# Performance work log

Measured on AMD Instinct MI355X. Metric: run time of the kernel, lower is better.

## Reference

```python
import jax, jax.numpy as jnp
import numpy as np

B, S, D = 2, 2048, 1024
H = 16
HD = D // H
RANK = 8
ALPHA = 8.0
NEG = -1e9


def setup_inputs() -> dict:
    key = jax.random.key(0)
    ks = jax.random.split(key, 7)
    inv = 1.0 / np.sqrt(D)
    return {
        "x": jax.random.normal(ks[0], (B, S, D), dtype=jnp.float32),
        "W_qkv": jax.random.normal(ks[1], (D, 3 * D), dtype=jnp.float32) * inv,
        "b_qkv": jax.random.normal(ks[2], (3 * D,), dtype=jnp.float32) * 0.02,
        # LoRA: A ~ N(0, 1/rank) per torch init; B is zeros at init but given
        # small values here so the LoRA path is exercised numerically.
        "A_lora": jax.random.normal(ks[3], (D, RANK), dtype=jnp.float32) / np.sqrt(RANK),
        "B_lora": jax.random.normal(ks[4], (RANK, 3 * D), dtype=jnp.float32) * 0.02,
        "W_proj": jax.random.normal(ks[5], (D, D), dtype=jnp.float32) * inv,
        "b_proj": jax.random.normal(ks[6], (D,), dtype=jnp.float32) * 0.02,
    }


def _split_heads(t):
    # [B, S, D] -> [B, H, S, HD]
    return t.reshape(B, S, H, HD).transpose(0, 2, 1, 3)


def reference(x, W_qkv, b_qkv, A_lora, B_lora, W_proj, b_proj):
    # c_attn: LoRALayer -> base linear + alpha * (x @ A @ B)
    qkv = x @ W_qkv + b_qkv + (x @ A_lora @ B_lora) * ALPHA  # [B, S, 3D]
    q, k, v = jnp.split(qkv, 3, axis=-1)
    q, k, v = _split_heads(q), _split_heads(k), _split_heads(v)

    # SelfAttentionFunction: QK^T, add mask, THEN divide by sqrt(head_dim)
    causal = jnp.tril(jnp.ones((S, S), dtype=bool))
    mask = jnp.where(causal, 0.0, NEG).astype(x.dtype)  # [S, S] additive
    scores = (jnp.einsum("bhqd,bhkd->bhqk", q, k) + mask) / jnp.sqrt(
        jnp.asarray(HD, dtype=x.dtype)
    )
    attn = jax.nn.softmax(scores, axis=-1)  # [B, H, S, S]
    ctx = jnp.einsum("bhqk,bhkd->bhqd", attn, v)  # [B, H, S, HD]

    # merge heads -> c_proj (plain LoRaLinear: x @ W + b)
    ctx = ctx.transpose(0, 2, 1, 3).reshape(B, S, D)
    out = ctx @ W_proj + b_proj
    return out
```

## Files before the change

kernel.cpp:

```cpp
#include <hip/hip_runtime.h>
#include <hip/hip_bf16.h>


#define BB    2
#define SS    2048
#define DD    1024
#define HH    16
#define HDIM  64
#define N3    3072
#define MR    4096

typedef short short8 __attribute__((ext_vector_type(8)));
typedef short s16x4 __attribute__((ext_vector_type(4)));
typedef float f32x4 __attribute__((ext_vector_type(4)));

#define MFMA16(a, b, c) __builtin_amdgcn_mfma_f32_16x16x32_bf16((a), (b), (c), 0, 0, 0)

__device__ __forceinline__ float b2f(short s) {
    union { unsigned int u; float f; } c;
    c.u = ((unsigned int)(unsigned short)s) << 16;
    return c.f;
}
__device__ __forceinline__ short f2b(float f) {
    union { __hip_bfloat16 h; short s; } c;
    c.h = __float2bfloat16(f);
    return c.s;
}
struct HiLo { short hi, lo; };
__device__ __forceinline__ HiLo split2(float v) {
    HiLo r;
    r.hi = f2b(v);
    r.lo = f2b(v - b2f(r.hi));
    return r;
}

__device__ __forceinline__ void gl_lds16(const void* g, void* l) {
    __builtin_amdgcn_global_load_lds(
        (const __attribute__((address_space(1))) void*)g,
        (__attribute__((address_space(3))) void*)l, 16, 0, 0);
}


__global__ __launch_bounds__(256) void split_x(const float* __restrict__ X,
                                               short* __restrict__ Xhi,
                                               short* __restrict__ Xlo) {
    int kc = blockIdx.x, p = blockIdx.y;
    int tid = threadIdx.x;
    int row = tid >> 1, half = tid & 1;
    const float* src = &X[((size_t)p * 128 + row) * 1024 + kc * 32 + half * 16];
    f32x4 v[4];
#pragma unroll
    for (int u = 0; u < 4; u++) v[u] = *(const f32x4*)(src + u * 4);
    size_t base = ((size_t)p * 32 + kc) * 4096 + (size_t)(half * 2) * 1024 + row * 8;
#pragma unroll
    for (int u = 0; u < 2; u++) {
        short8 h8, l8;
#pragma unroll
        for (int j = 0; j < 8; j++) {
            HiLo hl = split2(v[u * 2 + (j >> 2)][j & 3]);
            h8[j] = hl.hi; l8[j] = hl.lo;
        }
        *(short8*)&Xhi[base + u * 1024] = h8;
        *(short8*)&Xlo[base + u * 1024] = l8;
    }
}

__global__ __launch_bounds__(256) void prep_kernel(
    const float* __restrict__ W, const float* __restrict__ Al,
    const float* __restrict__ Bl, short* __restrict__ Whi,
    short* __restrict__ Wlo, int N, int lora)
{
    __shared__ float sw[64][68];
    __shared__ float sa[64][8];
    __shared__ float sb[8][64];
    int tid = threadIdx.x;
    int n0 = blockIdx.x * 64, k0 = blockIdx.y * 64;
#pragma unroll
    for (int p = 0; p < 4; p++) {
        int idx = p * 256 + tid;
        int kr = idx >> 4, ch = idx & 15;
        *(f32x4*)&sw[kr][ch * 4] = *(const f32x4*)&W[(size_t)(k0 + kr) * N + n0 + ch * 4];
    }
    if (lora) {
        if (tid < 64) {
#pragma unroll
            for (int r = 0; r < 8; r++) sa[tid][r] = Al[(k0 + tid) * 8 + r];
        } else if (tid < 128) {
            int c = tid - 64;
#pragma unroll
            for (int r = 0; r < 8; r++) sb[r][c] = Bl[(size_t)r * N + n0 + c];
        }
    }
    __syncthreads();
#pragma unroll
    for (int p = 0; p < 2; p++) {
        int idx = p * 256 + tid;
        int nr = idx >> 3, ch = idx & 7;
        short8 h8, l8;
#pragma unroll
        for (int j = 0; j < 8; j++) {
            int k = ch * 8 + j;
            float v = sw[k][nr];
            if (lora) {
                float a2 = 0.f;
#pragma unroll
                for (int r = 0; r < 8; r++) a2 += sa[k][r] * sb[r][nr];
                v += 8.0f * a2;
            }
            HiLo hl = split2(v);
            h8[j] = hl.hi;
            l8[j] = hl.lo;
        }
        int n = n0 + nr;
        int kchunk = (k0 >> 5) + (ch >> 2);
        size_t off = ((size_t)(n >> 7) * 32 + kchunk) * 4096 +
                     (size_t)(ch & 3) * 1024 + (n & 127) * 8;
        *(short8*)&Whi[off] = h8;
        *(short8*)&Wlo[off] = l8;
    }
}

__global__ __launch_bounds__(256) void gemm3(
    const short* __restrict__ Ahi, const short* __restrict__ Alo,
    const short* __restrict__ Bhi, const short* __restrict__ Blo,
    const float* __restrict__ bias,
    float* __restrict__ qf, short* __restrict__ khi, short* __restrict__ klo,
    short* __restrict__ vt, float* __restrict__ outf32, int N, int mode)
{
    __shared__ short lds[4][4][128][8];
    int tid = threadIdx.x;
    int wav = tid >> 6, lane = tid & 63;
    int l15 = lane & 15, q4 = lane >> 4;
    int wm = wav & 1, wn = wav >> 1;
    int n0 = blockIdx.x * 128, m0 = blockIdx.y * 128;

    const short* ga_h = Ahi + ((size_t)blockIdx.y * 32) * 4096 + tid * 8;
    const short* ga_l = Alo + ((size_t)blockIdx.y * 32) * 4096 + tid * 8;
    const short* gb_h = Bhi + ((size_t)blockIdx.x * 32) * 4096 + tid * 8;
    const short* gb_l = Blo + ((size_t)blockIdx.x * 32) * 4096 + tid * 8;
    short* l0 = &lds[0][0][0][0] + tid * 8;

    f32x4 acc[4][4] = {};

    for (int kc = 0; kc < 32; ++kc) {
        __syncthreads();
        int koff = kc * 4096;
        gl_lds16(ga_h + koff,        l0);
        gl_lds16(ga_h + koff + 2048, l0 + 2048);
        gl_lds16(ga_l + koff,        l0 + 4096);
        gl_lds16(ga_l + koff + 2048, l0 + 6144);
        gl_lds16(gb_h + koff,        l0 + 8192);
        gl_lds16(gb_h + koff + 2048, l0 + 10240);
        gl_lds16(gb_l + koff,        l0 + 12288);
        gl_lds16(gb_l + koff + 2048, l0 + 14336);
        __syncthreads();
        short8 ah[4], al_[4], bh[4], bl[4];
#pragma unroll
        for (int i = 0; i < 4; i++) {
            ah[i]  = *(short8*)&lds[0][q4][wm * 64 + i * 16 + l15][0];
            al_[i] = *(short8*)&lds[1][q4][wm * 64 + i * 16 + l15][0];
            bh[i]  = *(short8*)&lds[2][q4][wn * 64 + i * 16 + l15][0];
            bl[i]  = *(short8*)&lds[3][q4][wn * 64 + i * 16 + l15][0];
        }
#pragma unroll
        for (int mi = 0; mi < 4; mi++)
#pragma unroll
            for (int ni = 0; ni < 4; ni++) {
                acc[mi][ni] = MFMA16(ah[mi], bh[ni], acc[mi][ni]);
                acc[mi][ni] = MFMA16(ah[mi], bl[ni], acc[mi][ni]);
                acc[mi][ni] = MFMA16(al_[mi], bh[ni], acc[mi][ni]);
            }
    }
#pragma unroll
    for (int ni = 0; ni < 4; ni++) {
        int n = n0 + wn * 64 + ni * 16 + l15;
        float bv = bias[n];
#pragma unroll
        for (int mi = 0; mi < 4; mi++) {
            int mbase = m0 + wm * 64 + mi * 16 + q4 * 4;
#pragma unroll
            for (int r = 0; r < 4; r++) {
                int m = mbase + r;
                float v = acc[mi][ni][r] + bv;
                if (mode != 0) {
                    outf32[(size_t)m * 1024 + n] = v;
                } else if (n0 < 1024) {
                    qf[(size_t)m * 1024 + n] = v * 0.125f;
                } else if (n0 < 2048) {
                    int kk = n - 1024, hh = kk >> 6, hd = kk & 63;
                    int bb_ = m >> 11, s = m & 2047;
                    int oct = hd >> 3;
                    size_t base = ((size_t)((bb_ << 4) + hh) * 32 + (s >> 6)) * 4096
                                  + (size_t)oct * 512 + ((s & 63) ^ oct) * 8 + (hd & 7);
                    HiLo hl = split2(v);
                    khi[base] = hl.hi;
                    klo[base] = hl.lo;
                } else {
                    int kk = n - 2048, hh = kk >> 6, hd = kk & 63;
                    int bb_ = m >> 11, s = m & 2047;
                    int oct = (s >> 3) & 7;
                    size_t base = ((size_t)((bb_ << 4) + hh) * 32 + (s >> 6)) * 4096
                                  + (size_t)oct * 512 + (hd ^ oct) * 8 + (s & 7);
                    vt[base] = f2b(v);
                }
            }
        }
    }
}

__global__ __launch_bounds__(256) void attn_mfma(const float* __restrict__ qf,
                                                 const short* __restrict__ khi,
                                                 const short* __restrict__ klo,
                                                 const short* __restrict__ vtg,
                                                 short* __restrict__ ctxhi,
                                                 short* __restrict__ ctxlo) {
    __shared__ short KhL[2][4096];
    __shared__ short KlL[2][4096];
    __shared__ short VtL[2][4096];
    __shared__ short Pt[4][8][17][8];

    int h = blockIdx.y, b = blockIdx.z;
    int tid = threadIdx.x, wav = tid >> 6, lane = tid & 63;
    int l15 = lane & 15, q4 = lane >> 4;
    const float* bq = qf + (size_t)b * SS * 1024;
    size_t hb = (size_t)((b * 16 + h) * 32) * 4096;
    const short* gkh = khi + hb;
    const short* gkl = klo + hb;
    const short* gvt = vtg + hb;
    int t8 = tid * 8;

#define ISSUE(c, buf)                                                   \
    {                                                                   \
        size_t co_ = (size_t)(c) * 4096 + t8;                           \
        gl_lds16(gkh + co_,        &KhL[buf][t8]);                      \
        gl_lds16(gkh + co_ + 2048, &KhL[buf][t8 + 2048]);               \
        gl_lds16(gkl + co_,        &KlL[buf][t8]);                      \
        gl_lds16(gkl + co_ + 2048, &KlL[buf][t8 + 2048]);               \
        gl_lds16(gvt + co_,        &VtL[buf][t8]);                      \
        gl_lds16(gvt + co_ + 2048, &VtL[buf][t8 + 2048]);               \
    }

    for (int t = 0; t < 2; ++t) {
        int qt = t ? (int)blockIdx.x : 31 - (int)blockIdx.x;
        int qb = qt * 64;

        size_t qoff = (size_t)(qb + wav * 16 + l15) * 1024 + h * 64;
        short8 q0h, q0l, q1h, q1l;
        {
            f32x4 a0 = *(const f32x4*)&bq[qoff + q4 * 8];
            f32x4 a1 = *(const f32x4*)&bq[qoff + q4 * 8 + 4];
            f32x4 c0 = *(const f32x4*)&bq[qoff + 32 + q4 * 8];
            f32x4 c1 = *(const f32x4*)&bq[qoff + 32 + q4 * 8 + 4];
#pragma unroll
            for (int j = 0; j < 4; j++) {
                HiLo u = split2(a0[j]); q0h[j] = u.hi; q0l[j] = u.lo;
                HiLo v = split2(a1[j]); q0h[4 + j] = v.hi; q0l[4 + j] = v.lo;
                HiLo w = split2(c0[j]); q1h[j] = w.hi; q1l[j] = w.lo;
                HiLo z = split2(c1[j]); q1h[4 + j] = z.hi; q1l[4 + j] = z.lo;
            }
        }

        f32x4 o[4] = {};
        float msc = -1e30f;
        float lsc = 0.f;
        int nch = qt + 1;

        ISSUE(0, 0);
        __syncthreads();

        for (int c = 0; c < nch; ++c) {
            int cur = c & 1;
            int k0 = c * 64;

            if (c + 1 < nch) ISSUE(c + 1, cur ^ 1);

            f32x4 s[4];
            __builtin_amdgcn_s_setprio(1);
#pragma unroll
            for (int g = 0; g < 4; g++) {
                int ko  = q4 * 512 + ((g * 16 + l15) ^ q4) * 8;
                int ko2 = (4 + q4) * 512 + ((g * 16 + l15) ^ (4 + q4)) * 8;
                short8 k0h_ = *(short8*)&KhL[cur][ko];
                short8 k0l_ = *(short8*)&KlL[cur][ko];
                short8 k1h_ = *(short8*)&KhL[cur][ko2];
                short8 k1l_ = *(short8*)&KlL[cur][ko2];
                f32x4 acc = {};
                acc = MFMA16(k0h_, q0h, acc);
                acc = MFMA16(k0l_, q0h, acc);
                acc = MFMA16(k0h_, q0l, acc);
                acc = MFMA16(k1h_, q1h, acc);
                acc = MFMA16(k1l_, q1h, acc);
                acc = MFMA16(k1h_, q1l, acc);
                s[g] = acc;
            }
            __builtin_amdgcn_s_setprio(0);

            if (c == qt) {
                int q = qb + wav * 16 + l15;
#pragma unroll
                for (int g = 0; g < 4; g++)
#pragma unroll
                    for (int r = 0; r < 4; r++)
                        if (k0 + g * 16 + q4 * 4 + r > q) s[g][r] = -1e30f;
            }
            f32x4 mx4 = s[0];
#pragma unroll
            for (int g = 1; g < 4; g++) {
                mx4[0] = fmaxf(mx4[0], s[g][0]); mx4[1] = fmaxf(mx4[1], s[g][1]);
                mx4[2] = fmaxf(mx4[2], s[g][2]); mx4[3] = fmaxf(mx4[3], s[g][3]);
            }
            float mx = fmaxf(fmaxf(mx4[0], mx4[1]), fmaxf(mx4[2], mx4[3]));
            mx = fmaxf(mx, __shfl_xor(mx, 16, 64));
            mx = fmaxf(mx, __shfl_xor(mx, 32, 64));
            float mn = fmaxf(msc, mx);
            f32x4 ps = {};
#pragma unroll
            for (int g = 0; g < 4; g++) {
                s16x4 pb;
#pragma unroll
                for (int r = 0; r < 4; r++) {
                    float p = __expf(s[g][r] - mn);
                    ps[r] += p;
                    pb[r] = f2b(p);
                }
                *(s16x4*)&Pt[wav][g * 2 + (q4 >> 1)][l15][(q4 & 1) * 4] = pb;
            }
            float sm = (ps[0] + ps[1]) + (ps[2] + ps[3]);
            sm += __shfl_xor(sm, 16, 64);
            sm += __shfl_xor(sm, 32, 64);
            float alpha_s = __expf(msc - mn);
            msc = mn;
            lsc = lsc * alpha_s + sm;
            float al0 = __shfl(alpha_s, q4 * 4 + 0, 64);
            float al1 = __shfl(alpha_s, q4 * 4 + 1, 64);
            float al2 = __shfl(alpha_s, q4 * 4 + 2, 64);
            float al3 = __shfl(alpha_s, q4 * 4 + 3, 64);

            short8 pf0 = *(short8*)&Pt[wav][q4][l15][0];
            short8 pf1 = *(short8*)&Pt[wav][4 + q4][l15][0];
            __builtin_amdgcn_s_setprio(1);
#pragma unroll
            for (int gg = 0; gg < 4; gg++) {
                int vo  = q4 * 512 + ((gg * 16 + l15) ^ q4) * 8;
                int vo2 = (4 + q4) * 512 + ((gg * 16 + l15) ^ (4 + q4)) * 8;
                short8 vf0 = *(short8*)&VtL[cur][vo];
                short8 vf1 = *(short8*)&VtL[cur][vo2];
                f32x4 tt = o[gg];
                tt[0] *= al0; tt[1] *= al1; tt[2] *= al2; tt[3] *= al3;
                tt = MFMA16(pf0, vf0, tt);
                tt = MFMA16(pf1, vf1, tt);
                o[gg] = tt;
            }
            __builtin_amdgcn_s_setprio(0);

            __syncthreads();
        }

        float ls0 = __shfl(lsc, q4 * 4 + 0, 64);
        float ls1 = __shfl(lsc, q4 * 4 + 1, 64);
        float ls2 = __shfl(lsc, q4 * 4 + 2, 64);
        float ls3 = __shfl(lsc, q4 * 4 + 3, 64);
        float lsr[4] = {ls0, ls1, ls2, ls3};
#pragma unroll
        for (int gg = 0; gg < 4; gg++)
#pragma unroll
            for (int r = 0; r < 4; r++) {
                int q = qb + wav * 16 + q4 * 4 + r;
                int mrow = b * SS + q;
                int k = h * 64 + gg * 16 + l15;
                HiLo hl = split2(o[gg][r] / lsr[r]);
                size_t off = ((size_t)(mrow >> 7) * 32 + (k >> 5)) * 4096 +
                             (size_t)((k >> 3) & 3) * 1024 + (mrow & 127) * 8 + (k & 7);
                ctxhi[off] = hl.hi;
                ctxlo[off] = hl.lo;
            }
    }
#undef ISSUE
}

extern "C" void kernel_launch(void* const* d_in, const int* in_sizes, int n_in,
                              void* d_out, int out_size, void* d_ws, size_t ws_size,
                              hipStream_t stream) {
    const float* x  = (const float*)d_in[0];
    const float* Wq = (const float*)d_in[1];
    const float* bq = (const float*)d_in[2];
    const float* Al = (const float*)d_in[3];
    const float* Bl = (const float*)d_in[4];
    const float* Wp = (const float*)d_in[5];
    const float* bp = (const float*)d_in[6];

    char* ws = (char*)d_ws;
    float* qf     = (float*)(ws);
    short* khi    = (short*)(ws + (size_t)16 * 1024 * 1024);
    short* klo    = (short*)(ws + (size_t)24 * 1024 * 1024);
    short* vt     = (short*)(ws + (size_t)32 * 1024 * 1024);
    short* wpt_hi = (short*)(ws + (size_t)40 * 1024 * 1024);
    short* wpt_lo = (short*)(ws + (size_t)42 * 1024 * 1024);
    short* wqt_hi = (short*)(ws + (size_t)44 * 1024 * 1024);
    short* wqt_lo = (short*)(ws + (size_t)50 * 1024 * 1024);
    short* xhi    = (short*)(ws + (size_t)56 * 1024 * 1024);
    short* xlo    = (short*)(ws + (size_t)64 * 1024 * 1024);
    short* ctxhi  = (short*)(ws + (size_t)44 * 1024 * 1024);
    short* ctxlo  = (short*)(ws + (size_t)52 * 1024 * 1024);

    hipLaunchKernelGGL(split_x, dim3(32, 32), dim3(256), 0, stream, x, xhi, xlo);
    hipLaunchKernelGGL(prep_kernel, dim3(N3 / 64, 16), dim3(256), 0, stream,
                       Wq, Al, Bl, wqt_hi, wqt_lo, N3, 1);
    hipLaunchKernelGGL(prep_kernel, dim3(DD / 64, 16), dim3(256), 0, stream,
                       Wp, (const float*)nullptr, (const float*)nullptr,
                       wpt_hi, wpt_lo, DD, 0);
    hipLaunchKernelGGL(gemm3, dim3(N3 / 128, MR / 128), dim3(256), 0, stream,
                       xhi, xlo, wqt_hi, wqt_lo, bq,
                       qf, khi, klo, vt, (float*)nullptr, N3, 0);
    hipLaunchKernelGGL(attn_mfma, dim3(SS / 128, HH, BB), dim3(256), 0, stream,
                       qf, khi, klo, vt, ctxhi, ctxlo);
    hipLaunchKernelGGL(gemm3, dim3(DD / 128, MR / 128), dim3(256), 0, stream,
                       ctxhi, ctxlo, wpt_hi, wpt_lo, bp,
                       (float*)nullptr, (short*)nullptr, (short*)nullptr,
                       (short*)nullptr, (float*)d_out, DD, 1);
}
```

Before: 300.4 us.

## Double-buffer LDS tiles in split-bf16 GEMM to overlap loads with MFMA

The GEMM kernel now keeps two LDS buffers. The global-to-LDS loads for the next K chunk are issued before the MFMA work on the current chunk, and one barrier per iteration replaces the previous two. This aims to hide global memory latency behind the three-pass bf16 MFMA compute. In exchange, LDS use per block doubles to 64 KB, which may reduce the number of blocks resident per CU.

```diff
diff --git a/kernel.cpp b/kernel.cpp
--- a/kernel.cpp
+++ b/kernel.cpp
@@ -127,7 +127,7 @@
     float* __restrict__ qf, short* __restrict__ khi, short* __restrict__ klo,
     short* __restrict__ vt, float* __restrict__ outf32, int N, int mode)
 {
-    __shared__ short lds[4][4][128][8];
+    __shared__ short lds[2][4][4][128][8];
     int tid = threadIdx.x;
     int wav = tid >> 6, lane = tid & 63;
     int l15 = lane & 15, q4 = lane >> 4;
@@ -138,29 +138,37 @@
     const short* ga_l = Alo + ((size_t)blockIdx.y * 32) * 4096 + tid * 8;
     const short* gb_h = Bhi + ((size_t)blockIdx.x * 32) * 4096 + tid * 8;
     const short* gb_l = Blo + ((size_t)blockIdx.x * 32) * 4096 + tid * 8;
-    short* l0 = &lds[0][0][0][0] + tid * 8;
+    short* l0 = &lds[0][0][0][0][0] + tid * 8;
 
     f32x4 acc[4][4] = {};
 
+#define STAGE(kc_, buf_)                                         \
+    {                                                            \
+        int koff_ = (kc_) * 4096;                                \
+        short* lb_ = l0 + (buf_) * 16384;                        \
+        gl_lds16(ga_h + koff_,        lb_);                      \
+        gl_lds16(ga_h + koff_ + 2048, lb_ + 2048);               \
+        gl_lds16(ga_l + koff_,        lb_ + 4096);               \
+        gl_lds16(ga_l + koff_ + 2048, lb_ + 6144);               \
+        gl_lds16(gb_h + koff_,        lb_ + 8192);               \
+        gl_lds16(gb_h + koff_ + 2048, lb_ + 10240);              \
+        gl_lds16(gb_l + koff_,        lb_ + 12288);              \
+        gl_lds16(gb_l + koff_ + 2048, lb_ + 14336);              \
+    }
+
+    STAGE(0, 0);
+    __syncthreads();
+
     for (int kc = 0; kc < 32; ++kc) {
-        __syncthreads();
-        int koff = kc * 4096;
-        gl_lds16(ga_h + koff,        l0);
-        gl_lds16(ga_h + koff + 2048, l0 + 2048);
-        gl_lds16(ga_l + koff,        l0 + 4096);
-        gl_lds16(ga_l + koff + 2048, l0 + 6144);
-        gl_lds16(gb_h + koff,        l0 + 8192);
-        gl_lds16(gb_h + koff + 2048, l0 + 10240);
-        gl_lds16(gb_l + koff,        l0 + 12288);
-        gl_lds16(gb_l + koff + 2048, l0 + 14336);
-        __syncthreads();
+        int cur = kc & 1;
+        if (kc + 1 < 32) STAGE(kc + 1, cur ^ 1);
         short8 ah[4], al_[4], bh[4], bl[4];
 #pragma unroll
         for (int i = 0; i < 4; i++) {
-            ah[i]  = *(short8*)&lds[0][q4][wm * 64 + i * 16 + l15][0];
-            al_[i] = *(short8*)&lds[1][q4][wm * 64 + i * 16 + l15][0];
-            bh[i]  = *(short8*)&lds[2][q4][wn * 64 + i * 16 + l15][0];
-            bl[i]  = *(short8*)&lds[3][q4][wn * 64 + i * 16 + l15][0];
+            ah[i]  = *(short8*)&lds[cur][0][q4][wm * 64 + i * 16 + l15][0];
+            al_[i] = *(short8*)&lds[cur][1][q4][wm * 64 + i * 16 + l15][0];
+            bh[i]  = *(short8*)&lds[cur][2][q4][wn * 64 + i * 16 + l15][0];
+            bl[i]  = *(short8*)&lds[cur][3][q4][wn * 64 + i * 16 + l15][0];
         }
 #pragma unroll
         for (int mi = 0; mi < 4; mi++)
@@ -170,7 +178,9 @@
                 acc[mi][ni] = MFMA16(ah[mi], bl[ni], acc[mi][ni]);
                 acc[mi][ni] = MFMA16(al_[mi], bh[ni], acc[mi][ni]);
             }
-    }
+        __syncthreads();
+    }
+#undef STAGE
 #pragma unroll
     for (int ni = 0; ni < 4; ni++) {
         int n = n0 + wn * 64 + ni * 16 + l15;
```

Measured after the change: 279.0 us. 1.08x faster.
